# Optimization experiments

Measured on AMD Instinct MI355X. Metric: run time of the kernel, lower is better.

Reference implementation:

```python
import jax, jax.numpy as jnp
import numpy as np

N = 50000       # num_entities / nodes
E = 100000      # edges
K = 8           # incoming edge-graph neighbors per edge
D_NODE = 64
D_EDGE = 64
H = 4
DH = D_EDGE // H
DIN = D_EDGE + 2 * D_NODE  # [edge_feat, node_feat[src], node_feat[dst]]


def setup_inputs() -> dict:
    key = jax.random.key(0)
    ks = jax.random.split(key, 6)
    node_features = jax.random.normal(ks[0], (N, D_NODE), jnp.float32)
    edge_features = jax.random.normal(ks[1], (E, D_EDGE), jnp.float32)
    edge_index = jax.random.randint(ks[2], (2, E), 0, N)
    node_tiers = jax.random.randint(ks[3], (N,), 0, 4, dtype=jnp.int32)
    # edge adjacency (line graph): each edge attends to K other edges
    adj_dst = jnp.repeat(jnp.arange(E), K)                       # [A]
    adj_src = jax.random.randint(ks[4], (E * K,), 0, E)          # [A]
    # learned params: two EdgeAttention layers, each Wq/Wk/Wv [DIN,D_EDGE], Wo [D_EDGE,D_EDGE]
    wkeys = jax.random.split(ks[5], 8)
    def w(k, fan_in, fan_out):
        return jax.random.normal(k, (fan_in, fan_out), jnp.float32) * np.float32(1.0 / np.sqrt(fan_in))
    params = {}
    for li in (1, 2):
        base = (li - 1) * 4
        params[f'l{li}_Wq'] = w(wkeys[base + 0], DIN, D_EDGE)
        params[f'l{li}_Wk'] = w(wkeys[base + 1], DIN, D_EDGE)
        params[f'l{li}_Wv'] = w(wkeys[base + 2], DIN, D_EDGE)
        params[f'l{li}_Wo'] = w(wkeys[base + 3], D_EDGE, D_EDGE)
    return dict(node_features=node_features, edge_features=edge_features,
                edge_index=edge_index, node_tiers=node_tiers,
                adj_src=adj_src, adj_dst=adj_dst, **params)


def _edge_attention(node_f, edge_f, edge_index, adj_src, adj_dst, Wq, Wk, Wv, Wo):
    # x: edge feature conditioned on endpoint node features  [E, DIN]
    x = jnp.concatenate([edge_f, node_f[edge_index[0]], node_f[edge_index[1]]], axis=-1)
    q = (x @ Wq).reshape(E, H, DH)
    k = (x @ Wk).reshape(E, H, DH)
    v = (x @ Wv).reshape(E, H, DH)
    scale = np.float32(1.0 / np.sqrt(DH))
    # scores per adjacency pair  [A, H]
    s = jnp.einsum('ahd,ahd->ah', q[adj_dst], k[adj_src]) * scale
    # segment softmax over incoming neighbors of each dst edge
    m = jax.ops.segment_max(s, adj_dst, num_segments=E)          # [E, H]
    e = jnp.exp(s - m[adj_dst])                                   # [A, H]
    denom = jax.ops.segment_sum(e, adj_dst, num_segments=E)      # [E, H]
    alpha = e / denom[adj_dst]                                    # [A, H]
    out = jax.ops.segment_sum(alpha[..., None] * v[adj_src], adj_dst, num_segments=E)  # [E,H,DH]
    return edge_f + out.reshape(E, D_EDGE) @ Wo                   # residual


def reference(node_features, edge_features, edge_index, node_tiers, adj_src, adj_dst,
              l1_Wq, l1_Wk, l1_Wv, l1_Wo, l2_Wq, l2_Wk, l2_Wv, l2_Wo):
    ef = _edge_attention(node_features, edge_features, edge_index, adj_src, adj_dst,
                         l1_Wq, l1_Wk, l1_Wv, l1_Wo)
    ef = _edge_attention(node_features, ef, edge_index, adj_src, adj_dst,
                         l2_Wq, l2_Wk, l2_Wv, l2_Wo)
    return ef  # updated edge features of the output DeltaGraph
```

## Files before the change

kernel.cpp:

```cpp
#include <hip/hip_runtime.h>

#define NE 100000
#define NN 50000

typedef short short8 __attribute__((ext_vector_type(8)));
typedef float f32x4 __attribute__((ext_vector_type(4)));
typedef unsigned short ushort;
typedef unsigned int uint;

__device__ inline ushort f2bf(float f) {
    unsigned int u = __float_as_uint(f);
    u += 0x7FFFu + ((u >> 16) & 1u);
    return (ushort)(u >> 16);
}
__device__ inline float bf2f(ushort u) {
    return __uint_as_float((unsigned int)u << 16);
}

__device__ inline short8 pack_bf8(float4 a, float4 b) {
    short8 r;
    r[0] = (short)f2bf(a.x); r[1] = (short)f2bf(a.y);
    r[2] = (short)f2bf(a.z); r[3] = (short)f2bf(a.w);
    r[4] = (short)f2bf(b.x); r[5] = (short)f2bf(b.y);
    r[6] = (short)f2bf(b.z); r[7] = (short)f2bf(b.w);
    return r;
}

__device__ inline void pack_qkv_slot(int slot, const float* Wq, const float* Wk,
                                     const float* Wv, ushort* wf)
{
    int lane = slot & 63;
    int st = slot >> 6;
    int s = st / 12, t = st % 12;
    int n = t * 16 + (lane & 15);
    int kb = s * 32 + (lane >> 4) * 8;
    const float* w = (n < 64) ? Wq : (n < 128) ? Wk : Wv;
    int nn = n & 63;
    #pragma unroll
    for (int j = 0; j < 8; ++j)
        wf[(size_t)slot * 8 + j] = f2bf(w[(size_t)(kb + j) * 64 + nn]);
}

__device__ inline void pack_wo_slot(int slot, const float* Wo, ushort* wf)
{
    int lane = slot & 63;
    int st = slot >> 6;
    int s = st / 4, t = st % 4;
    int n = t * 16 + (lane & 15);
    int kb = s * 32 + (lane >> 4) * 8;
    #pragma unroll
    for (int j = 0; j < 8; ++j)
        wf[(size_t)slot * 8 + j] = f2bf(Wo[(size_t)(kb + j) * 64 + n]);
}

__global__ __launch_bounds__(256) void prep_all(
    const float* __restrict__ l1Wq, const float* __restrict__ l1Wk,
    const float* __restrict__ l1Wv, const float* __restrict__ l1Wo,
    const float* __restrict__ l2Wq, const float* __restrict__ l2Wk,
    const float* __restrict__ l2Wv, const float* __restrict__ l2Wo,
    ushort* __restrict__ wf1, ushort* __restrict__ wf2,
    ushort* __restrict__ wo1, ushort* __restrict__ wo2)
{
    int idx = blockIdx.x * 256 + threadIdx.x;
    if (idx < 4608)            pack_qkv_slot(idx,         l1Wq, l1Wk, l1Wv, wf1);
    else if (idx < 9216)       pack_qkv_slot(idx - 4608,  l2Wq, l2Wk, l2Wv, wf2);
    else if (idx < 9728)       pack_wo_slot (idx - 9216,  l1Wo, wo1);
    else if (idx < 10240)      pack_wo_slot (idx - 9728,  l2Wo, wo2);
}

__global__ __launch_bounds__(256, 3) void qkv_mfma(
    const float* __restrict__ ef, const float* __restrict__ nodef,
    const int* __restrict__ eidx, const ushort* __restrict__ wfrag,
    ushort* __restrict__ qo, ushort* __restrict__ ko, ushort* __restrict__ vo)
{
    __shared__ __align__(16) ushort lds_a[32 * 200];

    const int tid = threadIdx.x;
    const int l   = tid & 63;
    const int w   = tid >> 6;

    short8 Bf[6][3];
    #pragma unroll
    for (int s = 0; s < 6; ++s)
        #pragma unroll
        for (int n = 0; n < 3; ++n)
            Bf[s][n] = *(const short8*)((const char*)wfrag +
                        (size_t)((s * 12 + 3 * w + n) * 64 + l) * 16);

    {
        const int r   = tid >> 3;
        const int p   = tid & 7;
        const int row = blockIdx.x * 32 + r;
        const int rc  = (row < NE) ? row : NE - 1;
        const float* srcs[3] = { ef    + (size_t)rc * 64,
                                 nodef + (size_t)eidx[rc] * 64,
                                 nodef + (size_t)eidx[NE + rc] * 64 };
        #pragma unroll
        for (int c = 0; c < 3; ++c) {
            const float* sp = srcs[c] + p * 8;
            float4 f0 = *(const float4*)(sp + 0);
            float4 f1 = *(const float4*)(sp + 4);
            *(short8*)(lds_a + r * 200 + c * 64 + p * 8) = pack_bf8(f0, f1);
        }
    }

    f32x4 acc[2][3];
    #pragma unroll
    for (int T = 0; T < 2; ++T)
        #pragma unroll
        for (int n = 0; n < 3; ++n) acc[T][n] = (f32x4)(0.f);

    __syncthreads();

    const int rr = l & 15;
    const int kg = l >> 4;
    #pragma unroll
    for (int s = 0; s < 6; ++s) {
        short8 Af[2];
        #pragma unroll
        for (int T = 0; T < 2; ++T)
            Af[T] = *(const short8*)(lds_a + (T * 16 + rr) * 200 + s * 32 + kg * 8);
        #pragma unroll
        for (int T = 0; T < 2; ++T)
            #pragma unroll
            for (int n = 0; n < 3; ++n)
                acc[T][n] = __builtin_amdgcn_mfma_f32_16x16x32_bf16(
                                Af[T], Bf[s][n], acc[T][n], 0, 0, 0);
    }

    const int e0 = blockIdx.x * 32;
    #pragma unroll
    for (int T = 0; T < 2; ++T) {
        #pragma unroll
        for (int n = 0; n < 3; ++n) {
            const int c = (3 * w + n) * 16 + rr;
            ushort* dst = (c < 64) ? (qo + c) : (c < 128) ? (ko + (c - 64))
                                              : (vo + (c - 128));
            #pragma unroll
            for (int jj = 0; jj < 4; ++jj) {
                const int row = e0 + T * 16 + kg * 4 + jj;
                if (row < NE) dst[(size_t)row * 64] = f2bf(acc[T][n][jj]);
            }
        }
    }
}

__global__ __launch_bounds__(256) void attn_kernel(
    const ushort* __restrict__ q, const ushort* __restrict__ kbuf,
    const ushort* __restrict__ vbuf, const int* __restrict__ adj_src,
    ushort* __restrict__ ao)
{
    const int wid  = (blockIdx.x * 256 + threadIdx.x) >> 6;
    const int lane = threadIdx.x & 63;
    if (wid >= NE) return;
    const int e    = wid;
    const int half = lane >> 5;
    const int l32  = lane & 31;

    const int4 nb = *(const int4*)(adj_src + e * 8 + half * 4);
    const int nbr[4] = { nb.x, nb.y, nb.z, nb.w };

    ushort2 qu = *(const ushort2*)(q + (size_t)e * 64 + l32 * 2);
    const float q0 = bf2f(qu.x), q1 = bf2f(qu.y);

    ushort2 ku[4], vu[4];
    #pragma unroll
    for (int t = 0; t < 4; ++t) {
        ku[t] = *(const ushort2*)(kbuf + (size_t)nbr[t] * 64 + l32 * 2);
        vu[t] = *(const ushort2*)(vbuf + (size_t)nbr[t] * 64 + l32 * 2);
    }

    float s[4];
    #pragma unroll
    for (int t = 0; t < 4; ++t) {
        float p = q0 * bf2f(ku[t].x) + q1 * bf2f(ku[t].y);
        p += __shfl_xor(p, 1);
        p += __shfl_xor(p, 2);
        p += __shfl_xor(p, 4);
        s[t] = p * 0.25f;
    }

    float m = fmaxf(fmaxf(s[0], s[1]), fmaxf(s[2], s[3]));
    m = fmaxf(m, __shfl_xor(m, 32));
    float wgt[4], den = 0.f;
    #pragma unroll
    for (int t = 0; t < 4; ++t) { wgt[t] = __expf(s[t] - m); den += wgt[t]; }
    den += __shfl_xor(den, 32);
    const float inv = 1.f / den;

    float ox = 0.f, oy = 0.f;
    #pragma unroll
    for (int t = 0; t < 4; ++t) {
        ox = fmaf(wgt[t], bf2f(vu[t].x), ox);
        oy = fmaf(wgt[t], bf2f(vu[t].y), oy);
    }
    ox = (ox + __shfl_xor(ox, 32)) * inv;
    oy = (oy + __shfl_xor(oy, 32)) * inv;

    if (lane < 32) {
        ushort2 o;
        o.x = f2bf(ox);
        o.y = f2bf(oy);
        *(ushort2*)(ao + (size_t)e * 64 + l32 * 2) = o;
    }
}

__global__ __launch_bounds__(256) void wo_mfma(
    const float* __restrict__ ef_in, const ushort* __restrict__ attn,
    const ushort* __restrict__ wofrag, float* __restrict__ efo)
{
    const int wave = threadIdx.x >> 6;
    const int lane = threadIdx.x & 63;
    const int r  = lane & 15;
    const int kg = lane >> 4;
    const int e0 = blockIdx.x * 64 + wave * 16;
    const int e  = e0 + r;
    const int ec = (e < NE) ? e : NE - 1;

    short8 afr[2];
    #pragma unroll
    for (int s = 0; s < 2; ++s)
        afr[s] = *(const short8*)(attn + (size_t)ec * 64 + s * 32 + kg * 8);

    const short8* wf = (const short8*)wofrag;
    f32x4 acc[4];
    #pragma unroll
    for (int t = 0; t < 4; ++t) acc[t] = (f32x4)(0.f);
    #pragma unroll
    for (int s = 0; s < 2; ++s) {
        #pragma unroll
        for (int t = 0; t < 4; ++t) {
            short8 b = wf[(size_t)(s * 4 + t) * 64 + lane];
            acc[t] = __builtin_amdgcn_mfma_f32_16x16x32_bf16(afr[s], b, acc[t], 0, 0, 0);
        }
    }

    const int orow = e0 + kg * 4;
    #pragma unroll
    for (int t = 0; t < 4; ++t) {
        const int c = t * 16 + r;
        #pragma unroll
        for (int j = 0; j < 4; ++j) {
            int row = orow + j;
            if (row < NE) {
                size_t off = (size_t)row * 64 + c;
                efo[off] = acc[t][j] + ef_in[off];
            }
        }
    }
}

extern "C" void kernel_launch(void* const* d_in, const int* in_sizes, int n_in,
                              void* d_out, int out_size, void* d_ws, size_t ws_size,
                              hipStream_t stream)
{
    const float* nodef   = (const float*)d_in[0];
    const float* ef      = (const float*)d_in[1];
    const int*   eidx    = (const int*)d_in[2];
    const int*   adj_src = (const int*)d_in[4];
    const float* l1Wq = (const float*)d_in[6];
    const float* l1Wk = (const float*)d_in[7];
    const float* l1Wv = (const float*)d_in[8];
    const float* l1Wo = (const float*)d_in[9];
    const float* l2Wq = (const float*)d_in[10];
    const float* l2Wk = (const float*)d_in[11];
    const float* l2Wv = (const float*)d_in[12];
    const float* l2Wo = (const float*)d_in[13];

    ushort* q  = (ushort*)d_ws;
    ushort* k  = q  + (size_t)NE * 64;
    ushort* v  = k  + (size_t)NE * 64;
    ushort* ao = v  + (size_t)NE * 64;
    ushort* wf1 = ao + (size_t)NE * 64;
    ushort* wf2 = wf1 + 36864;
    ushort* wo1 = wf2 + 36864;
    ushort* wo2 = wo1 + 4096;
    float* out = (float*)d_out;

    dim3 blk(256);
    const int gq = (NE + 31) / 32;
    const int ga = (NE + 3) / 4;
    const int gw = (NE + 63) / 64;

    prep_all<<<40, blk, 0, stream>>>(l1Wq, l1Wk, l1Wv, l1Wo,
                                     l2Wq, l2Wk, l2Wv, l2Wo,
                                     wf1, wf2, wo1, wo2);

    qkv_mfma<<<gq, blk, 0, stream>>>(ef, nodef, eidx, wf1, q, k, v);
    attn_kernel<<<ga, blk, 0, stream>>>(q, k, v, adj_src, ao);
    wo_mfma<<<gw, blk, 0, stream>>>(ef, ao, wo1, out);
    qkv_mfma<<<gq, blk, 0, stream>>>(out, nodef, eidx, wf2, q, k, v);
    attn_kernel<<<ga, blk, 0, stream>>>(q, k, v, adj_src, ao);
    wo_mfma<<<gw, blk, 0, stream>>>(out, ao, wo2, out);
}
```

Baseline: 142.3 us.

## Restructure QKV projection: direct-to-register A rows, LDS-staged weights via global_load_lds

The QKV kernel now gives each wave its own 16 rows and computes all 192 output columns. A operands are loaded from global memory straight into registers instead of going through a shared LDS tile. Weight fragments are streamed into LDS in three phases with global_load_lds, and the block size grows to 64 rows, which halves the grid. The attention and Wo kernels get manual unrolling with no change in logic. The aim is to cut the per-block weight register load and LDS A-tile traffic, at the cost of extra barriers and serialized weight staging.

```diff
diff --git a/kernel.cpp b/kernel.cpp
--- a/kernel.cpp
+++ b/kernel.cpp
@@ -68,81 +68,112 @@
     else if (idx < 10240)      pack_wo_slot (idx - 9728,  l2Wo, wo2);
 }
 
-__global__ __launch_bounds__(256, 3) void qkv_mfma(
+#define MFMA_B16(a, b, c) c = __builtin_amdgcn_mfma_f32_16x16x32_bf16(a, b, c, 0, 0, 0)
+
+#define GLP const __attribute__((address_space(1))) uint*
+#define LDP __attribute__((address_space(3))) uint*
+
+#define STAGE(ph) do {                                                         \
+    const char* gs_ = (const char*)wfrag + (size_t)(ph) * 24576 + (size_t)l * 16; \
+    __builtin_amdgcn_global_load_lds((GLP)(gs_ + (size_t)(w*6+0)*1024), (LDP)(ldsb + (size_t)(w*6+0)*1024), 16, 0, 0); \
+    __builtin_amdgcn_global_load_lds((GLP)(gs_ + (size_t)(w*6+1)*1024), (LDP)(ldsb + (size_t)(w*6+1)*1024), 16, 0, 0); \
+    __builtin_amdgcn_global_load_lds((GLP)(gs_ + (size_t)(w*6+2)*1024), (LDP)(ldsb + (size_t)(w*6+2)*1024), 16, 0, 0); \
+    __builtin_amdgcn_global_load_lds((GLP)(gs_ + (size_t)(w*6+3)*1024), (LDP)(ldsb + (size_t)(w*6+3)*1024), 16, 0, 0); \
+    __builtin_amdgcn_global_load_lds((GLP)(gs_ + (size_t)(w*6+4)*1024), (LDP)(ldsb + (size_t)(w*6+4)*1024), 16, 0, 0); \
+    __builtin_amdgcn_global_load_lds((GLP)(gs_ + (size_t)(w*6+5)*1024), (LDP)(ldsb + (size_t)(w*6+5)*1024), 16, 0, 0); \
+} while (0)
+
+#define KSTEP(Areg, si) do {                                                   \
+    const char* lb_ = ldsb + (size_t)(si) * 12288 + (size_t)l * 16;            \
+    short8 b0_  = *(const short8*)(lb_ + 0);                                   \
+    short8 b1_  = *(const short8*)(lb_ + 1024);                                \
+    short8 b2_  = *(const short8*)(lb_ + 2048);                                \
+    short8 b3_  = *(const short8*)(lb_ + 3072);                                \
+    short8 b4_  = *(const short8*)(lb_ + 4096);                                \
+    short8 b5_  = *(const short8*)(lb_ + 5120);                                \
+    short8 b6_  = *(const short8*)(lb_ + 6144);                                \
+    short8 b7_  = *(const short8*)(lb_ + 7168);                                \
+    short8 b8_  = *(const short8*)(lb_ + 8192);                                \
+    short8 b9_  = *(const short8*)(lb_ + 9216);                                \
+    short8 b10_ = *(const short8*)(lb_ + 10240);                               \
+    short8 b11_ = *(const short8*)(lb_ + 11264);                               \
+    MFMA_B16(Areg, b0_,  c0);  MFMA_B16(Areg, b1_,  c1);                       \
+    MFMA_B16(Areg, b2_,  c2);  MFMA_B16(Areg, b3_,  c3);                       \
+    MFMA_B16(Areg, b4_,  c4);  MFMA_B16(Areg, b5_,  c5);                       \
+    MFMA_B16(Areg, b6_,  c6);  MFMA_B16(Areg, b7_,  c7);                       \
+    MFMA_B16(Areg, b8_,  c8);  MFMA_B16(Areg, b9_,  c9);                       \
+    MFMA_B16(Areg, b10_, c10); MFMA_B16(Areg, b11_, c11);                      \
+} while (0)
+
+#define STORE_T(creg, dstp, cloc) do {                                         \
+    ushort* dp_ = (dstp) + (cloc);                                             \
+    int row_ = e0 + kg * 4;                                                    \
+    if (row_ + 0 < NE) dp_[(size_t)(row_ + 0) * 64] = f2bf(creg[0]);           \
+    if (row_ + 1 < NE) dp_[(size_t)(row_ + 1) * 64] = f2bf(creg[1]);           \
+    if (row_ + 2 < NE) dp_[(size_t)(row_ + 2) * 64] = f2bf(creg[2]);           \
+    if (row_ + 3 < NE) dp_[(size_t)(row_ + 3) * 64] = f2bf(creg[3]);           \
+} while (0)
+
+__global__ __launch_bounds__(256) void qkv_mfma(
     const float* __restrict__ ef, const float* __restrict__ nodef,
     const int* __restrict__ eidx, const ushort* __restrict__ wfrag,
     ushort* __restrict__ qo, ushort* __restrict__ ko, ushort* __restrict__ vo)
 {
-    __shared__ __align__(16) ushort lds_a[32 * 200];
+    __shared__ __align__(1024) char ldsb[24 * 1024];
 
     const int tid = threadIdx.x;
     const int l   = tid & 63;
     const int w   = tid >> 6;
-
-    short8 Bf[6][3];
-    #pragma unroll
-    for (int s = 0; s < 6; ++s)
-        #pragma unroll
-        for (int n = 0; n < 3; ++n)
-            Bf[s][n] = *(const short8*)((const char*)wfrag +
-                        (size_t)((s * 12 + 3 * w + n) * 64 + l) * 16);
-
-    {
-        const int r   = tid >> 3;
-        const int p   = tid & 7;
-        const int row = blockIdx.x * 32 + r;
-        const int rc  = (row < NE) ? row : NE - 1;
-        const float* srcs[3] = { ef    + (size_t)rc * 64,
-                                 nodef + (size_t)eidx[rc] * 64,
-                                 nodef + (size_t)eidx[NE + rc] * 64 };
-        #pragma unroll
-        for (int c = 0; c < 3; ++c) {
-            const float* sp = srcs[c] + p * 8;
-            float4 f0 = *(const float4*)(sp + 0);
-            float4 f1 = *(const float4*)(sp + 4);
-            *(short8*)(lds_a + r * 200 + c * 64 + p * 8) = pack_bf8(f0, f1);
-        }
-    }
-
-    f32x4 acc[2][3];
-    #pragma unroll
-    for (int T = 0; T < 2; ++T)
-        #pragma unroll
-        for (int n = 0; n < 3; ++n) acc[T][n] = (f32x4)(0.f);
-
-    __syncthreads();
-
-    const int rr = l & 15;
-    const int kg = l >> 4;
-    #pragma unroll
-    for (int s = 0; s < 6; ++s) {
-        short8 Af[2];
-        #pragma unroll
-        for (int T = 0; T < 2; ++T)
-            Af[T] = *(const short8*)(lds_a + (T * 16 + rr) * 200 + s * 32 + kg * 8);
-        #pragma unroll
-        for (int T = 0; T < 2; ++T)
-            #pragma unroll
-            for (int n = 0; n < 3; ++n)
-                acc[T][n] = __builtin_amdgcn_mfma_f32_16x16x32_bf16(
-                                Af[T], Bf[s][n], acc[T][n], 0, 0, 0);
-    }
-
-    const int e0 = blockIdx.x * 32;
-    #pragma unroll
-    for (int T = 0; T < 2; ++T) {
-        #pragma unroll
-        for (int n = 0; n < 3; ++n) {
-            const int c = (3 * w + n) * 16 + rr;
-            ushort* dst = (c < 64) ? (qo + c) : (c < 128) ? (ko + (c - 64))
-                                              : (vo + (c - 128));
-            #pragma unroll
-            for (int jj = 0; jj < 4; ++jj) {
-                const int row = e0 + T * 16 + kg * 4 + jj;
-                if (row < NE) dst[(size_t)row * 64] = f2bf(acc[T][n][jj]);
-            }
-        }
-    }
+    const int r   = l & 15;
+    const int kg  = l >> 4;
+    const int e0  = blockIdx.x * 64 + w * 16;
+    const int e   = e0 + r;
+    const int ec  = (e < NE) ? e : NE - 1;
+
+    STAGE(0);
+
+    const int koff = kg * 8;
+    const float* rp0 = ef    + (size_t)ec * 64;
+    const float* rp1 = nodef + (size_t)eidx[ec] * 64;
+    const float* rp2 = nodef + (size_t)eidx[NE + ec] * 64;
+
+    short8 A0 = pack_bf8(*(const float4*)(rp0 + koff),      *(const float4*)(rp0 + koff + 4));
+    short8 A1 = pack_bf8(*(const float4*)(rp0 + 32 + koff), *(const float4*)(rp0 + 36 + koff));
+    short8 A2 = pack_bf8(*(const float4*)(rp1 + koff),      *(const float4*)(rp1 + koff + 4));
+    short8 A3 = pack_bf8(*(const float4*)(rp1 + 32 + koff), *(const float4*)(rp1 + 36 + koff));
+    short8 A4 = pack_bf8(*(const float4*)(rp2 + koff),      *(const float4*)(rp2 + koff + 4));
+    short8 A5 = pack_bf8(*(const float4*)(rp2 + 32 + koff), *(const float4*)(rp2 + 36 + koff));
+
+    f32x4 c0 = (f32x4)(0.f), c1 = (f32x4)(0.f), c2  = (f32x4)(0.f), c3  = (f32x4)(0.f);
+    f32x4 c4 = (f32x4)(0.f), c5 = (f32x4)(0.f), c6  = (f32x4)(0.f), c7  = (f32x4)(0.f);
+    f32x4 c8 = (f32x4)(0.f), c9 = (f32x4)(0.f), c10 = (f32x4)(0.f), c11 = (f32x4)(0.f);
+
+    __syncthreads();
+    KSTEP(A0, 0);
+    KSTEP(A1, 1);
+    __syncthreads();
+    STAGE(1);
+    __syncthreads();
+    KSTEP(A2, 0);
+    KSTEP(A3, 1);
+    __syncthreads();
+    STAGE(2);
+    __syncthreads();
+    KSTEP(A4, 0);
+    KSTEP(A5, 1);
+
+    STORE_T(c0,  qo, 0 * 16 + r);
+    STORE_T(c1,  qo, 1 * 16 + r);
+    STORE_T(c2,  qo, 2 * 16 + r);
+    STORE_T(c3,  qo, 3 * 16 + r);
+    STORE_T(c4,  ko, 0 * 16 + r);
+    STORE_T(c5,  ko, 1 * 16 + r);
+    STORE_T(c6,  ko, 2 * 16 + r);
+    STORE_T(c7,  ko, 3 * 16 + r);
+    STORE_T(c8,  vo, 0 * 16 + r);
+    STORE_T(c9,  vo, 1 * 16 + r);
+    STORE_T(c10, vo, 2 * 16 + r);
+    STORE_T(c11, vo, 3 * 16 + r);
 }
 
 __global__ __launch_bounds__(256) void attn_kernel(
@@ -158,42 +189,43 @@
     const int l32  = lane & 31;
 
     const int4 nb = *(const int4*)(adj_src + e * 8 + half * 4);
-    const int nbr[4] = { nb.x, nb.y, nb.z, nb.w };
+    const int nbr0 = nb.x, nbr1 = nb.y, nbr2 = nb.z, nbr3 = nb.w;
 
     ushort2 qu = *(const ushort2*)(q + (size_t)e * 64 + l32 * 2);
     const float q0 = bf2f(qu.x), q1 = bf2f(qu.y);
 
-    ushort2 ku[4], vu[4];
-    #pragma unroll
-    for (int t = 0; t < 4; ++t) {
-        ku[t] = *(const ushort2*)(kbuf + (size_t)nbr[t] * 64 + l32 * 2);
-        vu[t] = *(const ushort2*)(vbuf + (size_t)nbr[t] * 64 + l32 * 2);
-    }
-
-    float s[4];
-    #pragma unroll
-    for (int t = 0; t < 4; ++t) {
-        float p = q0 * bf2f(ku[t].x) + q1 * bf2f(ku[t].y);
-        p += __shfl_xor(p, 1);
-        p += __shfl_xor(p, 2);
-        p += __shfl_xor(p, 4);
-        s[t] = p * 0.25f;
-    }
-
-    float m = fmaxf(fmaxf(s[0], s[1]), fmaxf(s[2], s[3]));
+    ushort2 ku0 = *(const ushort2*)(kbuf + (size_t)nbr0 * 64 + l32 * 2);
+    ushort2 ku1 = *(const ushort2*)(kbuf + (size_t)nbr1 * 64 + l32 * 2);
+    ushort2 ku2 = *(const ushort2*)(kbuf + (size_t)nbr2 * 64 + l32 * 2);
+    ushort2 ku3 = *(const ushort2*)(kbuf + (size_t)nbr3 * 64 + l32 * 2);
+    ushort2 vu0 = *(const ushort2*)(vbuf + (size_t)nbr0 * 64 + l32 * 2);
+    ushort2 vu1 = *(const ushort2*)(vbuf + (size_t)nbr1 * 64 + l32 * 2);
+    ushort2 vu2 = *(const ushort2*)(vbuf + (size_t)nbr2 * 64 + l32 * 2);
+    ushort2 vu3 = *(const ushort2*)(vbuf + (size_t)nbr3 * 64 + l32 * 2);
+
+    float s0 = q0 * bf2f(ku0.x) + q1 * bf2f(ku0.y);
+    float s1 = q0 * bf2f(ku1.x) + q1 * bf2f(ku1.y);
+    float s2 = q0 * bf2f(ku2.x) + q1 * bf2f(ku2.y);
+    float s3 = q0 * bf2f(ku3.x) + q1 * bf2f(ku3.y);
+    s0 += __shfl_xor(s0, 1); s0 += __shfl_xor(s0, 2); s0 += __shfl_xor(s0, 4);
+    s1 += __shfl_xor(s1, 1); s1 += __shfl_xor(s1, 2); s1 += __shfl_xor(s1, 4);
+    s2 += __shfl_xor(s2, 1); s2 += __shfl_xor(s2, 2); s2 += __shfl_xor(s2, 4);
+    s3 += __shfl_xor(s3, 1); s3 += __shfl_xor(s3, 2); s3 += __shfl_xor(s3, 4);
+    s0 *= 0.25f; s1 *= 0.25f; s2 *= 0.25f; s3 *= 0.25f;
+
+    float m = fmaxf(fmaxf(s0, s1), fmaxf(s2, s3));
     m = fmaxf(m, __shfl_xor(m, 32));
-    float wgt[4], den = 0.f;
-    #pragma unroll
-    for (int t = 0; t < 4; ++t) { wgt[t] = __expf(s[t] - m); den += wgt[t]; }
+    float w0 = __expf(s0 - m), w1 = __expf(s1 - m);
+    float w2 = __expf(s2 - m), w3 = __expf(s3 - m);
+    float den = w0 + w1 + w2 + w3;
     den += __shfl_xor(den, 32);
     const float inv = 1.f / den;
 
     float ox = 0.f, oy = 0.f;
-    #pragma unroll
-    for (int t = 0; t < 4; ++t) {
-        ox = fmaf(wgt[t], bf2f(vu[t].x), ox);
-        oy = fmaf(wgt[t], bf2f(vu[t].y), oy);
-    }
+    ox = fmaf(w0, bf2f(vu0.x), ox); oy = fmaf(w0, bf2f(vu0.y), oy);
+    ox = fmaf(w1, bf2f(vu1.x), ox); oy = fmaf(w1, bf2f(vu1.y), oy);
+    ox = fmaf(w2, bf2f(vu2.x), ox); oy = fmaf(w2, bf2f(vu2.y), oy);
+    ox = fmaf(w3, bf2f(vu3.x), ox); oy = fmaf(w3, bf2f(vu3.y), oy);
     ox = (ox + __shfl_xor(ox, 32)) * inv;
     oy = (oy + __shfl_xor(oy, 32)) * inv;
 
@@ -217,34 +249,35 @@
     const int e  = e0 + r;
     const int ec = (e < NE) ? e : NE - 1;
 
-    short8 afr[2];
-    #pragma unroll
-    for (int s = 0; s < 2; ++s)
-        afr[s] = *(const short8*)(attn + (size_t)ec * 64 + s * 32 + kg * 8);
-
-    const short8* wf = (const short8*)wofrag;
-    f32x4 acc[4];
-    #pragma unroll
-    for (int t = 0; t < 4; ++t) acc[t] = (f32x4)(0.f);
-    #pragma unroll
-    for (int s = 0; s < 2; ++s) {
-        #pragma unroll
-        for (int t = 0; t < 4; ++t) {
-            short8 b = wf[(size_t)(s * 4 + t) * 64 + lane];
-            acc[t] = __builtin_amdgcn_mfma_f32_16x16x32_bf16(afr[s], b, acc[t], 0, 0, 0);
-        }
-    }
+    short8 af0 = *(const short8*)(attn + (size_t)ec * 64 + kg * 8);
+    short8 af1 = *(const short8*)(attn + (size_t)ec * 64 + 32 + kg * 8);
+
+    const char* wf = (const char*)wofrag + (size_t)lane * 16;
+    f32x4 d0 = (f32x4)(0.f), d1 = (f32x4)(0.f), d2 = (f32x4)(0.f), d3 = (f32x4)(0.f);
+    short8 g0 = *(const short8*)(wf + 0 * 1024);
+    short8 g1 = *(const short8*)(wf + 1 * 1024);
+    short8 g2 = *(const short8*)(wf + 2 * 1024);
+    short8 g3 = *(const short8*)(wf + 3 * 1024);
+    MFMA_B16(af0, g0, d0); MFMA_B16(af0, g1, d1);
+    MFMA_B16(af0, g2, d2); MFMA_B16(af0, g3, d3);
+    g0 = *(const short8*)(wf + 4 * 1024);
+    g1 = *(const short8*)(wf + 5 * 1024);
+    g2 = *(const short8*)(wf + 6 * 1024);
+    g3 = *(const short8*)(wf + 7 * 1024);
+    MFMA_B16(af1, g0, d0); MFMA_B16(af1, g1, d1);
+    MFMA_B16(af1, g2, d2); MFMA_B16(af1, g3, d3);
 
     const int orow = e0 + kg * 4;
     #pragma unroll
     for (int t = 0; t < 4; ++t) {
+        const f32x4 dd = (t == 0) ? d0 : (t == 1) ? d1 : (t == 2) ? d2 : d3;
         const int c = t * 16 + r;
         #pragma unroll
         for (int j = 0; j < 4; ++j) {
             int row = orow + j;
             if (row < NE) {
                 size_t off = (size_t)row * 64 + c;
-                efo[off] = acc[t][j] + ef_in[off];
+                efo[off] = dd[j] + ef_in[off];
             }
         }
     }
@@ -278,7 +311,7 @@
     float* out = (float*)d_out;
 
     dim3 blk(256);
-    const int gq = (NE + 31) / 32;
+    const int gq = (NE + 63) / 64;
     const int ga = (NE + 3) / 4;
     const int gw = (NE + 63) / 64;
 
```

New measurement: 149.2 us. +4.9%, slower.
